# Kernel tuning notes

Hardware: AMD Instinct MI355X
Metric: run time of the kernel (lower is better)

## Reference

```python
import math
import jax, jax.numpy as jnp
import numpy as np

N_INPUTS, N_OUTPUTS = 2049, 1024
OUT_START, OUT_END, IN_END = 25.0, 24000.0, 24000.0


def _build_buffers(n_inputs=N_INPUTS, n_outputs=N_OUTPUTS, output_start=OUT_START,
                   output_end=OUT_END, input_end=IN_END):
    # Mirrors LogScale.__init__ (numpy, construction-time, exact).
    scale = 1.0
    min_log = math.log10(1.0 + scale * output_start)
    max_log = math.log10(1.0 + scale * output_end)
    lin_logs = np.linspace(min_log, max_log, n_outputs, dtype=np.float64)
    freq_per_bin = scale * float(input_end) / (n_inputs - 1)
    center_bins = ((np.power(10.0, lin_logs) - 1.0) / freq_per_bin).astype(np.float32)
    n_linear = 0
    while n_linear < n_outputs - 1 and (center_bins[n_linear + 1] - center_bins[n_linear] <= 1.0 or center_bins[n_linear] < 1.0):
        n_linear += 1
    output_start_idx = center_bins[:n_linear].astype(np.int64)
    fraction_linear = center_bins[:n_linear] - output_start_idx.astype(np.float32)
    linear_pair_idx = (np.concatenate([output_start_idx, output_start_idx + 1])
                       if n_linear > 0 else np.zeros(0, dtype=np.int64))
    n_sum = n_linear
    while n_sum < n_outputs - 2 and (center_bins[n_sum + 1] - center_bins[n_sum] <= 2.0 or center_bins[n_sum] < 2.0):
        n_sum += 1
    fraction_cubic = center_bins[n_linear:n_sum].copy()
    n_tri = n_outputs - n_sum
    ft = center_bins[n_sum:n_sum + n_tri]
    dt = center_bins[n_sum:n_sum + n_tri] - center_bins[n_sum - 1:n_sum - 1 + n_tri]
    weights = np.full((max(n_tri, 1), n_inputs), -np.inf, dtype=np.float32)
    for i in range(n_tri):
        i_mid = int(math.ceil(ft[i]))
        i_start = int(math.ceil(ft[i] - dt[i]))
        i_end = int(math.ceil(ft[i] + dt[i + 1])) if i < n_tri - 1 else i_mid
        weights[i, i_mid] = 0.0
        dist_left = float(i_mid - i_start)
        for ib in range(i_start + 1, i_mid):
            weights[i, ib] = np.float32(10.0 * np.log10(1.0 - (i_mid - ib) / dist_left))
        if i_end > i_mid:
            dist_right = float(i_end - i_mid)
            for ib in range(i_mid + 1, i_end):
                weights[i, ib] = np.float32(10.0 * np.log10(np.float32(1.0 - (ib - i_mid) / dist_right)))
    return linear_pair_idx, fraction_linear, fraction_cubic, weights[:n_tri]


def setup_inputs() -> dict:
    key = jax.random.key(0)
    x = jax.random.normal(key, (32, 512, N_INPUTS), dtype=jnp.float32)
    pidx, flin, fcub, w = _build_buffers()
    return {
        "x": x,
        "fraction_linear": jnp.asarray(flin),
        "fraction_cubic": jnp.asarray(fcub),
        "triangular_weights": jnp.asarray(w),
        "linear_pair_idx": jnp.asarray(pidx, dtype=jnp.int32),
    }


_TRI_CHUNK = 128  # rows of flattened x per lax.map step (bounds the dense intermediate)


def _tri_max(flat, w):
    # (x[:, None, :] + w).max(-1), chunked along N to keep the (chunk, n_tri, n_in)
    # intermediate bounded, mirroring the torch _triangular_amax chunking.
    n, n_in = flat.shape
    pad = (-n) % _TRI_CHUNK
    flat_p = jnp.pad(flat, ((0, pad), (0, 0)))
    xb = flat_p.reshape(-1, _TRI_CHUNK, n_in)
    out = jax.lax.map(lambda xc: jnp.max(xc[:, None, :] + w[None, :, :], axis=-1), xb)
    return out.reshape(-1, w.shape[0])[:n]


def _forward(x, fraction_linear, fraction_cubic, triangular_weights, linear_pair_idx):
    lead = x.shape[:-1]
    n_lin = fraction_linear.shape[0]
    outs = []
    if n_lin > 0:
        pair = jnp.take(x, linear_pair_idx, axis=-1).reshape(*lead, 2, n_lin)
        x0, x1 = pair[..., 0, :], pair[..., 1, :]
        outs.append(x0 + fraction_linear * (x1 - x0))
    if fraction_cubic.shape[0] > 0:
        i0 = jnp.floor(fraction_cubic).astype(jnp.int32)
        f = fraction_cubic - i0.astype(fraction_cubic.dtype)
        g = lambda off: jnp.take(x, i0 + off, axis=-1)
        xm1, xc0, xc1, xc2 = g(-1), g(0), g(1), g(2)
        # Catmull-Rom cubic interpolation at fractional position f in [0,1)
        cubic = xc0 + 0.5 * f * ((xc1 - xm1) + f * ((2.0 * xm1 - 5.0 * xc0 + 4.0 * xc1 - xc2)
                                                    + f * (3.0 * (xc0 - xc1) + xc2 - xm1)))
        outs.append(cubic)
    if triangular_weights.shape[0] > 0:
        flat = x.reshape(-1, x.shape[-1])
        outs.append(_tri_max(flat, triangular_weights).reshape(*lead, triangular_weights.shape[0]))
    return jnp.concatenate(outs, axis=-1)


def reference(x, fraction_linear, fraction_cubic, triangular_weights, linear_pair_idx):
    return _forward(x, fraction_linear, fraction_cubic, triangular_weights, linear_pair_idx)
```

## Files before the change

### kernel.cpp

```cpp
#include <hip/hip_runtime.h>
#include <math.h>

#define NI 2049
#define MAXW 64

__global__ void logscale_preproc(const float* __restrict__ w, int n_in,
                                 int* __restrict__ tri_start,
                                 int* __restrict__ tri_cnt,
                                 float* __restrict__ wpack) {
    const int i = blockIdx.x;
    __shared__ int smin, smax;
    if (threadIdx.x == 0) { smin = n_in; smax = -1; }
    __syncthreads();

    int lmin = n_in, lmax = -1;
    const float* wr = w + (size_t)i * n_in;
    for (int b = threadIdx.x; b < n_in; b += blockDim.x) {
        float v = wr[b];
        if (v > -1e30f) {
            lmin = min(lmin, b);
            lmax = max(lmax, b);
        }
    }
    atomicMin(&smin, lmin);
    atomicMax(&smax, lmax);
    __syncthreads();

    int s = smin;
    int cnt = smax - smin + 1;
    if (cnt > MAXW) cnt = MAXW;
    if (cnt < 1) { s = 0; cnt = 1; }
    if (threadIdx.x == 0) { tri_start[i] = s; tri_cnt[i] = cnt; }
    for (int j = threadIdx.x; j < MAXW; j += blockDim.x) {
        wpack[(size_t)i * MAXW + j] = (j < cnt) ? wr[s + j] : -INFINITY;
    }
}

__global__ __launch_bounds__(256) void logscale_main(
    const float* __restrict__ x,
    const float* __restrict__ flin,
    const float* __restrict__ fcub,
    const int*   __restrict__ pidx,
    const int*   __restrict__ tri_start,
    const int*   __restrict__ tri_cnt,
    const float* __restrict__ wpack,
    float* __restrict__ out,
    int n_lin, int n_cub, int n_tri) {

    const int row = blockIdx.x;
    __shared__ float lds[NI];

    const float* xr = x + (size_t)row * NI;
    for (int b = threadIdx.x; b < NI; b += blockDim.x) lds[b] = xr[b];
    __syncthreads();

    const int n_out = n_lin + n_cub + n_tri;
    float* orow = out + (size_t)row * n_out;

    for (int o = threadIdx.x; o < n_out; o += blockDim.x) {
        float r;
        if (o < n_lin) {
            const int i0 = pidx[o];
            const int i1 = pidx[n_lin + o];
            const float f = flin[o];
            const float x0 = lds[i0];
            const float x1 = lds[i1];
            r = x0 + f * (x1 - x0);
        } else if (o < n_lin + n_cub) {
            const int i = o - n_lin;
            const float c = fcub[i];
            const int i0 = (int)floorf(c);
            const float f = c - (float)i0;
            const float xm1 = lds[i0 - 1];
            const float x0  = lds[i0];
            const float x1  = lds[i0 + 1];
            const float x2  = lds[i0 + 2];
            r = x0 + 0.5f * f * (x1 - xm1 +
                    f * (2.0f * xm1 - 5.0f * x0 + 4.0f * x1 - x2 +
                    f * (3.0f * (x0 - x1) + x2 - xm1)));
        } else {
            const int i = o - n_lin - n_cub;
            const int s = tri_start[i];
            const int cnt = tri_cnt[i];
            const float* wp = wpack + (size_t)i * MAXW;
            float m = -INFINITY;
            for (int j = 0; j < cnt; ++j) {
                m = fmaxf(m, lds[s + j] + wp[j]);
            }
            r = m;
        }
        orow[o] = r;
    }
}

extern "C" void kernel_launch(void* const* d_in, const int* in_sizes, int n_in,
                              void* d_out, int out_size, void* d_ws, size_t ws_size,
                              hipStream_t stream) {
    (void)n_in; (void)ws_size;
    const float* x     = (const float*)d_in[0];
    const float* flin  = (const float*)d_in[1];
    const float* fcub  = (const float*)d_in[2];
    const float* w     = (const float*)d_in[3];
    const int*   pidx  = (const int*)d_in[4];
    float* out = (float*)d_out;

    const int n_lin  = in_sizes[1];
    const int n_cub  = in_sizes[2];
    const int n_tri  = in_sizes[3] / NI;
    const int n_rows = in_sizes[0] / NI;
    (void)out_size;

    int*   tri_start = (int*)d_ws;
    int*   tri_cnt   = tri_start + n_tri;
    float* wpack     = (float*)(tri_cnt + n_tri);

    if (n_tri > 0) {
        logscale_preproc<<<n_tri, 256, 0, stream>>>(w, NI, tri_start, tri_cnt, wpack);
    }
    logscale_main<<<n_rows, 256, 0, stream>>>(x, flin, fcub, pidx,
                                              tri_start, tri_cnt, wpack,
                                              out, n_lin, n_cub, n_tri);
}
```

Baseline: 320.0 us.

## Process four rows per block with packed per-output metadata and LDS-resident weights

Each block of the main kernel now loads four input rows into LDS and reuses one compacted per-output metadata table (float4 with indices and fractions) and one variable-length packed weight array staged in LDS, instead of separate global lookups per row. A new single-block pack kernel builds the metadata and prefix-summed weight offsets, which removes the fixed 64-wide weight padding. This is meant to amortize metadata and weight loads across rows and vectorize the row loads. In exchange it adds a third launch, a serial single-block prefix sum, and roughly 49KB of LDS per block, which lowers occupancy. Four rows per block also cuts the number of blocks.

Result: slower. 327.7 us (+2.4%).

```diff
diff --git a/kernel.cpp b/kernel.cpp
--- a/kernel.cpp
+++ b/kernel.cpp
@@ -2,122 +2,189 @@
 #include <math.h>
 
 #define NI 2049
-#define MAXW 64
+#define ROWS 4
+#define WCAP 4096
+#define NTRI_MAX 512
 
-__global__ void logscale_preproc(const float* __restrict__ w, int n_in,
-                                 int* __restrict__ tri_start,
-                                 int* __restrict__ tri_cnt,
-                                 float* __restrict__ wpack) {
+__global__ void logscale_win(const float* __restrict__ w, int n_in,
+                             int* __restrict__ tri_start,
+                             int* __restrict__ tri_cnt) {
     const int i = blockIdx.x;
     __shared__ int smin, smax;
     if (threadIdx.x == 0) { smin = n_in; smax = -1; }
     __syncthreads();
-
     int lmin = n_in, lmax = -1;
     const float* wr = w + (size_t)i * n_in;
     for (int b = threadIdx.x; b < n_in; b += blockDim.x) {
         float v = wr[b];
-        if (v > -1e30f) {
-            lmin = min(lmin, b);
-            lmax = max(lmax, b);
-        }
+        if (v > -1e30f) { lmin = min(lmin, b); lmax = max(lmax, b); }
     }
     atomicMin(&smin, lmin);
     atomicMax(&smax, lmax);
     __syncthreads();
+    if (threadIdx.x == 0) {
+        int s = smin, cnt = smax - smin + 1;
+        if (cnt < 1) { s = 0; cnt = 1; }
+        if (cnt > 64) cnt = 64;
+        tri_start[i] = s; tri_cnt[i] = cnt;
+    }
+}
 
-    int s = smin;
-    int cnt = smax - smin + 1;
-    if (cnt > MAXW) cnt = MAXW;
-    if (cnt < 1) { s = 0; cnt = 1; }
-    if (threadIdx.x == 0) { tri_start[i] = s; tri_cnt[i] = cnt; }
-    for (int j = threadIdx.x; j < MAXW; j += blockDim.x) {
-        wpack[(size_t)i * MAXW + j] = (j < cnt) ? wr[s + j] : -INFINITY;
+__global__ void logscale_pack(const float* __restrict__ w,
+                              const float* __restrict__ flin,
+                              const float* __restrict__ fcub,
+                              const int*   __restrict__ pidx,
+                              const int*   __restrict__ tri_start,
+                              const int*   __restrict__ tri_cnt,
+                              float4* __restrict__ meta,
+                              float*  __restrict__ wpk,
+                              int*    __restrict__ d_total,
+                              int n_lin, int n_cub, int n_tri) {
+    __shared__ int offs[NTRI_MAX + 1];
+    __shared__ int starts[NTRI_MAX];
+    const int tid = threadIdx.x;
+    for (int i = tid; i < n_tri; i += blockDim.x) {
+        offs[i + 1] = tri_cnt[i];
+        starts[i]   = tri_start[i];
+    }
+    __syncthreads();
+    if (tid == 0) {
+        offs[0] = 0;
+        for (int i = 1; i <= n_tri; ++i) offs[i] += offs[i - 1];
+        int t = offs[n_tri]; if (t > WCAP) t = WCAP;
+        *d_total = t;
+    }
+    __syncthreads();
+    int total = offs[n_tri]; if (total > WCAP) total = WCAP;
+
+    const int n_out = n_lin + n_cub + n_tri;
+    for (int o = tid; o < n_out; o += blockDim.x) {
+        float4 m;
+        if (o < n_lin) {
+            m.x = __int_as_float(pidx[o]);
+            m.y = __int_as_float(pidx[n_lin + o]);
+            m.z = flin[o]; m.w = 0.0f;
+        } else if (o < n_lin + n_cub) {
+            float c = fcub[o - n_lin];
+            int i0 = (int)floorf(c);
+            m.x = __int_as_float(i0);
+            m.y = 0.0f;
+            m.z = c - (float)i0; m.w = 0.0f;
+        } else {
+            int i = o - n_lin - n_cub;
+            int oa = min(offs[i], WCAP), ob = min(offs[i + 1], WCAP);
+            m.x = __int_as_float(starts[i]);
+            m.y = __int_as_float(ob - oa);
+            m.z = __int_as_float(oa); m.w = 0.0f;
+        }
+        meta[o] = m;
+    }
+    for (int p = tid; p < total; p += blockDim.x) {
+        int lo = 0, hi = n_tri - 1;
+        while (lo < hi) {
+            int mid = (lo + hi + 1) >> 1;
+            if (offs[mid] <= p) lo = mid; else hi = mid - 1;
+        }
+        int j = p - offs[lo];
+        wpk[p] = w[(size_t)lo * NI + starts[lo] + j];
     }
 }
 
 __global__ __launch_bounds__(256) void logscale_main(
-    const float* __restrict__ x,
-    const float* __restrict__ flin,
-    const float* __restrict__ fcub,
-    const int*   __restrict__ pidx,
-    const int*   __restrict__ tri_start,
-    const int*   __restrict__ tri_cnt,
-    const float* __restrict__ wpack,
+    const float*  __restrict__ x,
+    const float4* __restrict__ meta,
+    const float*  __restrict__ wpk,
+    const int*    __restrict__ d_total,
     float* __restrict__ out,
-    int n_lin, int n_cub, int n_tri) {
+    int n_lin, int n_cub, int n_out, int n_rows) {
 
-    const int row = blockIdx.x;
-    __shared__ float lds[NI];
+    __shared__ float xs[ROWS * NI];
+    __shared__ float wl[WCAP];
 
-    const float* xr = x + (size_t)row * NI;
-    for (int b = threadIdx.x; b < NI; b += blockDim.x) lds[b] = xr[b];
+    const int tid  = threadIdx.x;
+    const int row0 = blockIdx.x * ROWS;
+    const int rows_here = min(ROWS, n_rows - row0);
+
+    if (rows_here == ROWS) {
+        const float4* xc = (const float4*)(x + (size_t)row0 * NI);
+        for (int i = tid; i < (ROWS * NI) / 4; i += 256)
+            ((float4*)xs)[i] = xc[i];
+        if ((ROWS * NI) & 3) {  }
+    } else {
+        const float* xr = x + (size_t)row0 * NI;
+        for (int i = tid; i < rows_here * NI; i += 256) xs[i] = xr[i];
+    }
+    const int tw = *d_total;
+    for (int i = tid; i < tw; i += 256) wl[i] = wpk[i];
     __syncthreads();
 
-    const int n_out = n_lin + n_cub + n_tri;
-    float* orow = out + (size_t)row * n_out;
-
-    for (int o = threadIdx.x; o < n_out; o += blockDim.x) {
-        float r;
-        if (o < n_lin) {
-            const int i0 = pidx[o];
-            const int i1 = pidx[n_lin + o];
-            const float f = flin[o];
-            const float x0 = lds[i0];
-            const float x1 = lds[i1];
-            r = x0 + f * (x1 - x0);
-        } else if (o < n_lin + n_cub) {
-            const int i = o - n_lin;
-            const float c = fcub[i];
-            const int i0 = (int)floorf(c);
-            const float f = c - (float)i0;
-            const float xm1 = lds[i0 - 1];
-            const float x0  = lds[i0];
-            const float x1  = lds[i0 + 1];
-            const float x2  = lds[i0 + 2];
-            r = x0 + 0.5f * f * (x1 - xm1 +
-                    f * (2.0f * xm1 - 5.0f * x0 + 4.0f * x1 - x2 +
-                    f * (3.0f * (x0 - x1) + x2 - xm1)));
-        } else {
-            const int i = o - n_lin - n_cub;
-            const int s = tri_start[i];
-            const int cnt = tri_cnt[i];
-            const float* wp = wpack + (size_t)i * MAXW;
-            float m = -INFINITY;
-            for (int j = 0; j < cnt; ++j) {
-                m = fmaxf(m, lds[s + j] + wp[j]);
+    const int n_lc = n_lin + n_cub;
+    float* ob = out + (size_t)row0 * n_out;
+    for (int r = 0; r < rows_here; ++r) {
+        const float* xrow = xs + r * NI;
+        for (int o = tid; o < n_out; o += 256) {
+            float4 m = meta[o];
+            float res;
+            if (o < n_lin) {
+                const int i0 = __float_as_int(m.x);
+                const int i1 = __float_as_int(m.y);
+                const float f = m.z;
+                const float x0 = xrow[i0];
+                const float x1 = xrow[i1];
+                res = x0 + f * (x1 - x0);
+            } else if (o < n_lc) {
+                const int i0 = __float_as_int(m.x);
+                const float f = m.z;
+                const float xm1 = xrow[i0 - 1];
+                const float x0  = xrow[i0];
+                const float x1  = xrow[i0 + 1];
+                const float x2  = xrow[i0 + 2];
+                res = x0 + 0.5f * f * (x1 - xm1 +
+                        f * (2.0f * xm1 - 5.0f * x0 + 4.0f * x1 - x2 +
+                        f * (3.0f * (x0 - x1) + x2 - xm1)));
+            } else {
+                const int s   = __float_as_int(m.x);
+                const int cnt = __float_as_int(m.y);
+                const int off = __float_as_int(m.z);
+                float mx = -INFINITY;
+                #pragma unroll 4
+                for (int j = 0; j < cnt; ++j)
+                    mx = fmaxf(mx, xrow[s + j] + wl[off + j]);
+                res = mx;
             }
-            r = m;
+            ob[(size_t)r * n_out + o] = res;
         }
-        orow[o] = r;
     }
 }
 
 extern "C" void kernel_launch(void* const* d_in, const int* in_sizes, int n_in,
                               void* d_out, int out_size, void* d_ws, size_t ws_size,
                               hipStream_t stream) {
-    (void)n_in; (void)ws_size;
-    const float* x     = (const float*)d_in[0];
-    const float* flin  = (const float*)d_in[1];
-    const float* fcub  = (const float*)d_in[2];
-    const float* w     = (const float*)d_in[3];
-    const int*   pidx  = (const int*)d_in[4];
+    (void)n_in; (void)ws_size; (void)out_size;
+    const float* x    = (const float*)d_in[0];
+    const float* flin = (const float*)d_in[1];
+    const float* fcub = (const float*)d_in[2];
+    const float* w    = (const float*)d_in[3];
+    const int*   pidx = (const int*)d_in[4];
     float* out = (float*)d_out;
 
     const int n_lin  = in_sizes[1];
     const int n_cub  = in_sizes[2];
     const int n_tri  = in_sizes[3] / NI;
     const int n_rows = in_sizes[0] / NI;
-    (void)out_size;
+    const int n_out  = n_lin + n_cub + n_tri;
 
-    int*   tri_start = (int*)d_ws;
-    int*   tri_cnt   = tri_start + n_tri;
-    float* wpack     = (float*)(tri_cnt + n_tri);
+    float4* meta      = (float4*)d_ws;
+    float*  wpk       = (float*)(meta + n_out);
+    int*    tri_start = (int*)(wpk + WCAP);
+    int*    tri_cnt   = tri_start + NTRI_MAX;
+    int*    d_total   = tri_cnt + NTRI_MAX;
 
-    if (n_tri > 0) {
-        logscale_preproc<<<n_tri, 256, 0, stream>>>(w, NI, tri_start, tri_cnt, wpack);
-    }
-    logscale_main<<<n_rows, 256, 0, stream>>>(x, flin, fcub, pidx,
-                                              tri_start, tri_cnt, wpack,
-                                              out, n_lin, n_cub, n_tri);
+    if (n_tri > 0)
+        logscale_win<<<n_tri, 256, 0, stream>>>(w, NI, tri_start, tri_cnt);
+    logscale_pack<<<1, 256, 0, stream>>>(w, flin, fcub, pidx, tri_start, tri_cnt,
+                                         meta, wpk, d_total, n_lin, n_cub, n_tri);
+    const int nblk = (n_rows + ROWS - 1) / ROWS;
+    logscale_main<<<nblk, 256, 0, stream>>>(x, meta, wpk, d_total, out,
+                                            n_lin, n_cub, n_out, n_rows);
 }
```
